# Kernel optimization log

Measured on AMD Instinct MI355X. Metric: run time of the kernel, lower is better.

## Reference

```python
import jax, jax.numpy as jnp
import numpy as np

NODE_DIM = 256
EDGE_DIM = 128
HIDDEN = EDGE_DIM // 2  # edge_downsample=2 -> 64
LN_EPS = 1e-5


def setup_inputs() -> dict:
    key = jax.random.key(0)
    ks = jax.random.split(key, 12)
    B, N = 1, 768
    s_in = 1.0 / np.sqrt(NODE_DIM)
    s_h = 1.0 / np.sqrt(HIDDEN)
    return {
        "x": jax.random.normal(ks[0], (B, N, NODE_DIM), jnp.float32),
        "z": jnp.zeros((1,), jnp.float32),  # unused in forward (matches torch module)
        "Wi": jax.random.uniform(ks[1], (NODE_DIM, HIDDEN), jnp.float32, -s_in, s_in),
        "bi": jax.random.uniform(ks[2], (HIDDEN,), jnp.float32, -s_in, s_in),
        "Wj": jax.random.uniform(ks[3], (NODE_DIM, HIDDEN), jnp.float32, -s_in, s_in),
        "bj": jax.random.uniform(ks[4], (HIDDEN,), jnp.float32, -s_in, s_in),
        "ln_g": jnp.ones((HIDDEN,), jnp.float32),
        "ln_b": jnp.zeros((HIDDEN,), jnp.float32),
        "W1": jax.random.uniform(ks[5], (HIDDEN, HIDDEN), jnp.float32, -s_h, s_h),
        "b1": jax.random.uniform(ks[6], (HIDDEN,), jnp.float32, -s_h, s_h),
        "W2": jax.random.uniform(ks[7], (HIDDEN, EDGE_DIM), jnp.float32, -s_h, s_h),
        "b2": jax.random.uniform(ks[8], (EDGE_DIM,), jnp.float32, -s_h, s_h),
    }


def _layernorm(h, g, b):
    mu = jnp.mean(h, axis=-1, keepdims=True)
    var = jnp.mean(jnp.square(h - mu), axis=-1, keepdims=True)
    return (h - mu) * jax.lax.rsqrt(var + LN_EPS) * g + b


def reference(x, z, Wi, bi, Wj, bj, ln_g, ln_b, W1, b1, W2, b2):
    # x: [B, N, node_dim]
    n_i = x @ Wi + bi  # [B, N, H]
    n_j = x @ Wj + bj  # [B, N, H]
    # outer sum: [B, N(j-axis first per torch indexing), N, H]
    n_in = n_i[:, None, :, :] + n_j[:, :, None, :]
    h = _layernorm(n_in, ln_g, ln_b)
    h = jax.nn.relu(h @ W1 + b1)
    return h @ W2 + b2  # [B, N, N, edge_dim]
```

## Files before the change

### kernel.cpp

```cpp
#include <hip/hip_runtime.h>
#include <hip/hip_bf16.h>

typedef float f32x4 __attribute__((ext_vector_type(4)));
typedef short s16x8 __attribute__((ext_vector_type(8)));
typedef short s16x4 __attribute__((ext_vector_type(4)));

#define N_NODES 768
#define NODE_DIM_ 256
#define HDIM 64
#define EDIM 128
#define CTILES 48
#define TILES_TOTAL (N_NODES * CTILES)

static __device__ __forceinline__ short f2bf(float f) {
    __hip_bfloat16 h = __float2bfloat16(f);
    return __builtin_bit_cast(short, h);
}

__global__ __launch_bounds__(256) void proj_kernel(
        const float* __restrict__ x,
        const float* __restrict__ Wi, const float* __restrict__ bi,
        const float* __restrict__ Wj, const float* __restrict__ bj,
        float* __restrict__ NI, float* __restrict__ NJ) {
    int row  = blockIdx.x * 4 + (threadIdx.x >> 6);
    int lane = threadIdx.x & 63;
    float ai = bi[lane];
    float aj = bj[lane];
    const float* xr = x + row * NODE_DIM_;
#pragma unroll 8
    for (int k = 0; k < NODE_DIM_; ++k) {
        float xv = xr[k];
        ai = fmaf(xv, Wi[k * HDIM + lane], ai);
        aj = fmaf(xv, Wj[k * HDIM + lane], aj);
    }
    NI[row * HDIM + lane] = ai;
    NJ[row * HDIM + lane] = aj;
}

__global__ __launch_bounds__(256) void edge_kernel(
        const float* __restrict__ NI, const float* __restrict__ NJ,
        const float* __restrict__ lng, const float* __restrict__ lnb,
        const float* __restrict__ W1, const float* __restrict__ b1,
        const float* __restrict__ W2, const float* __restrict__ b2,
        float* __restrict__ out) {
    __shared__ short W1L[4096];
    __shared__ short W2L[8192];
    __shared__ short TL[4][1024];

    for (int idx = threadIdx.x; idx < 4096; idx += 256) {
        int k = idx >> 6, n = idx & 63;
        W1L[(k >> 3) * 512 + n * 8 + (k & 7)] = f2bf(W1[idx]);
    }
    for (int idx = threadIdx.x; idx < 8192; idx += 256) {
        int k = idx >> 7, n = idx & 127;
        W2L[(k >> 3) * 1024 + n * 8 + (k & 7)] = f2bf(W2[idx]);
    }
    __syncthreads();

    const int wave = threadIdx.x >> 6;
    const int lane = threadIdx.x & 63;
    const int l15  = lane & 15;
    const int hi   = lane >> 4;
    const int swz  = (l15 & 7) << 4;

    float gl[8], gh[8], bl[8], bh[8];
#pragma unroll
    for (int j = 0; j < 8; ++j) {
        gl[j] = lng[hi * 8 + j];      gh[j] = lng[32 + hi * 8 + j];
        bl[j] = lnb[hi * 8 + j];      bh[j] = lnb[32 + hi * 8 + j];
    }
    float b1v[16];
#pragma unroll
    for (int nt = 0; nt < 4; ++nt)
#pragma unroll
        for (int r = 0; r < 4; ++r)
            b1v[nt * 4 + r] = b1[nt * 16 + hi * 4 + r];
    float b2v[8];
#pragma unroll
    for (int nt = 0; nt < 8; ++nt)
        b2v[nt] = b2[nt * 16 + l15];

    char* tl = (char*)&TL[wave][0];

    const int wid = blockIdx.x * 4 + wave;
    const int nw  = gridDim.x * 4;
    for (int t = wid; t < TILES_TOTAL; t += nw) {
        int a  = t / CTILES;
        int c0 = (t - a * CTILES) * 16;

        const float* nip = NI + (c0 + l15) * HDIM + hi * 8;
        const float* njp = NJ + a * HDIM + hi * 8;
        float v[16];
#pragma unroll
        for (int j = 0; j < 8; ++j) {
            v[j]     = nip[j]      + njp[j];
            v[8 + j] = nip[32 + j] + njp[32 + j];
        }
        float s = 0.f, ss = 0.f;
#pragma unroll
        for (int j = 0; j < 16; ++j) { s += v[j]; ss = fmaf(v[j], v[j], ss); }
        s += __shfl_xor(s, 16);  ss += __shfl_xor(ss, 16);
        s += __shfl_xor(s, 32);  ss += __shfl_xor(ss, 32);
        float mu   = s * (1.f / 64.f);
        float var  = ss * (1.f / 64.f) - mu * mu;
        float rstd = rsqrtf(var + 1e-5f);

        s16x8 hf0, hf1;
#pragma unroll
        for (int j = 0; j < 8; ++j) {
            hf0[j] = f2bf(fmaf((v[j]     - mu) * rstd, gl[j], bl[j]));
            hf1[j] = f2bf(fmaf((v[8 + j] - mu) * rstd, gh[j], bh[j]));
        }

#pragma unroll
        for (int nt = 0; nt < 4; ++nt) {
            f32x4 acc = {0.f, 0.f, 0.f, 0.f};
            s16x8 w0 = *(const s16x8*)&W1L[(0 + hi) * 512 + (nt * 16 + l15) * 8];
            s16x8 w1 = *(const s16x8*)&W1L[(4 + hi) * 512 + (nt * 16 + l15) * 8];
            acc = __builtin_amdgcn_mfma_f32_16x16x32_bf16(w0, hf0, acc, 0, 0, 0);
            acc = __builtin_amdgcn_mfma_f32_16x16x32_bf16(w1, hf1, acc, 0, 0, 0);
            s16x4 tv;
#pragma unroll
            for (int r = 0; r < 4; ++r)
                tv[r] = f2bf(fmaxf(acc[r] + b1v[nt * 4 + r], 0.f));
            int wb = (l15 * 128 + (nt * 16 + hi * 4) * 2) ^ swz;
            *(s16x4*)(tl + wb) = tv;
        }

        int rb0 = (l15 * 128 + hi * 16) ^ swz;
        int rb1 = (l15 * 128 + hi * 16 + 64) ^ swz;
        s16x8 tf0 = *(const s16x8*)(tl + rb0);
        s16x8 tf1 = *(const s16x8*)(tl + rb1);

        float* op = out + ((size_t)(a * N_NODES + c0 + hi * 4)) * EDIM + l15;
#pragma unroll
        for (int nt = 0; nt < 8; ++nt) {
            f32x4 acc = {0.f, 0.f, 0.f, 0.f};
            s16x8 w0 = *(const s16x8*)&W2L[(0 + hi) * 1024 + (nt * 16 + l15) * 8];
            s16x8 w1 = *(const s16x8*)&W2L[(4 + hi) * 1024 + (nt * 16 + l15) * 8];
            acc = __builtin_amdgcn_mfma_f32_16x16x32_bf16(tf0, w0, acc, 0, 0, 0);
            acc = __builtin_amdgcn_mfma_f32_16x16x32_bf16(tf1, w1, acc, 0, 0, 0);
#pragma unroll
            for (int r = 0; r < 4; ++r)
                op[(size_t)r * EDIM + nt * 16] = acc[r] + b2v[nt];
        }
    }
}

extern "C" void kernel_launch(void* const* d_in, const int* in_sizes, int n_in,
                              void* d_out, int out_size, void* d_ws, size_t ws_size,
                              hipStream_t stream) {
    const float* x   = (const float*)d_in[0];
    const float* Wi  = (const float*)d_in[2];
    const float* bi  = (const float*)d_in[3];
    const float* Wj  = (const float*)d_in[4];
    const float* bj  = (const float*)d_in[5];
    const float* lng = (const float*)d_in[6];
    const float* lnb = (const float*)d_in[7];
    const float* W1  = (const float*)d_in[8];
    const float* b1  = (const float*)d_in[9];
    const float* W2  = (const float*)d_in[10];
    const float* b2  = (const float*)d_in[11];
    float* out = (float*)d_out;

    float* NI = (float*)d_ws;
    float* NJ = NI + N_NODES * HDIM;

    proj_kernel<<<N_NODES / 4, 256, 0, stream>>>(x, Wi, bi, Wj, bj, NI, NJ);
    edge_kernel<<<2304, 256, 0, stream>>>(NI, NJ, lng, lnb, W1, b1, W2, b2, out);
}
```

Before: 80.91 us.

## Fold LayerNorm and first linear layer into per-node precomputed projections

The first MLP layer after LayerNorm is rewritten algebraically. Per-node projections through gamma-scaled W1 (Pi, Pj), row means and second moments, and the column sums S1 and bias C1 are precomputed in the projection kernel. The edge kernel then gets mean and variance from per-node stats plus one dot product, and forms the hidden activations with a few FMAs. This removes the first MFMA stage, the LDS staging, and W1 loading. Each wave now owns a fixed column tile and iterates over 12 row tiles with 768 blocks. The risk is the numerical precision of computing variance from moments, and the kernel is still dominated by the large output write.

```diff
diff --git a/kernel.cpp b/kernel.cpp
--- a/kernel.cpp
+++ b/kernel.cpp
@@ -3,14 +3,13 @@
 
 typedef float f32x4 __attribute__((ext_vector_type(4)));
 typedef short s16x8 __attribute__((ext_vector_type(8)));
-typedef short s16x4 __attribute__((ext_vector_type(4)));
 
 #define N_NODES 768
 #define NODE_DIM_ 256
 #define HDIM 64
 #define EDIM 128
 #define CTILES 48
-#define TILES_TOTAL (N_NODES * CTILES)
+#define ATILES_PER_WAVE 12
 
 static __device__ __forceinline__ short f2bf(float f) {
     __hip_bfloat16 h = __float2bfloat16(f);
@@ -21,11 +20,23 @@
         const float* __restrict__ x,
         const float* __restrict__ Wi, const float* __restrict__ bi,
         const float* __restrict__ Wj, const float* __restrict__ bj,
-        float* __restrict__ NI, float* __restrict__ NJ) {
-    int row  = blockIdx.x * 4 + (threadIdx.x >> 6);
-    int lane = threadIdx.x & 63;
-    float ai = bi[lane];
-    float aj = bj[lane];
+        const float* __restrict__ W1, const float* __restrict__ b1,
+        const float* __restrict__ lng, const float* __restrict__ lnb,
+        float* __restrict__ NI, float* __restrict__ NJ,
+        float* __restrict__ Pi, float* __restrict__ Pj,
+        float* __restrict__ mi, float* __restrict__ qi,
+        float* __restrict__ mj, float* __restrict__ qj,
+        float* __restrict__ S1, float* __restrict__ C1) {
+    __shared__ float W1gL[HDIM * HDIM];
+    __shared__ float rowi[4][HDIM], rowj[4][HDIM];
+    for (int idx = threadIdx.x; idx < HDIM * HDIM; idx += 256) {
+        int k = idx >> 6;
+        W1gL[idx] = lng[k] * W1[idx];
+    }
+
+    int wave = threadIdx.x >> 6, lane = threadIdx.x & 63;
+    int row  = blockIdx.x * 4 + wave;
+    float ai = bi[lane], aj = bj[lane];
     const float* xr = x + row * NODE_DIM_;
 #pragma unroll 8
     for (int k = 0; k < NODE_DIM_; ++k) {
@@ -35,25 +46,56 @@
     }
     NI[row * HDIM + lane] = ai;
     NJ[row * HDIM + lane] = aj;
-}
-
-__global__ __launch_bounds__(256) void edge_kernel(
+    rowi[wave][lane] = ai;
+    rowj[wave][lane] = aj;
+
+    float si = ai, sqi = ai * ai, sj = aj, sqj = aj * aj;
+#pragma unroll
+    for (int o = 1; o < 64; o <<= 1) {
+        si  += __shfl_xor(si, o);   sqi += __shfl_xor(sqi, o);
+        sj  += __shfl_xor(sj, o);   sqj += __shfl_xor(sqj, o);
+    }
+    if (lane == 0) {
+        mi[row] = si * (1.f / 64.f);  qi[row] = sqi * (1.f / 64.f);
+        mj[row] = sj * (1.f / 64.f);  qj[row] = sqj * (1.f / 64.f);
+    }
+    __syncthreads();
+
+    float pi = 0.f, pj = 0.f;
+#pragma unroll 8
+    for (int k = 0; k < HDIM; ++k) {
+        float wg = W1gL[k * HDIM + lane];
+        pi = fmaf(rowi[wave][k], wg, pi);
+        pj = fmaf(rowj[wave][k], wg, pj);
+    }
+    Pi[row * HDIM + lane] = pi;
+    Pj[row * HDIM + lane] = pj;
+
+    if (blockIdx.x == 0 && threadIdx.x < HDIM) {
+        int n = threadIdx.x;
+        float s = 0.f, cc = 0.f;
+#pragma unroll 8
+        for (int k = 0; k < HDIM; ++k) {
+            s += W1gL[k * HDIM + n];
+            cc = fmaf(lnb[k], W1[k * HDIM + n], cc);
+        }
+        S1[n] = s;
+        C1[n] = cc + b1[n];
+    }
+}
+
+__global__ __launch_bounds__(256, 3) void edge_kernel(
         const float* __restrict__ NI, const float* __restrict__ NJ,
-        const float* __restrict__ lng, const float* __restrict__ lnb,
-        const float* __restrict__ W1, const float* __restrict__ b1,
+        const float* __restrict__ Pi, const float* __restrict__ Pj,
+        const float* __restrict__ mi, const float* __restrict__ qi,
+        const float* __restrict__ mj, const float* __restrict__ qj,
+        const float* __restrict__ S1, const float* __restrict__ C1,
         const float* __restrict__ W2, const float* __restrict__ b2,
         float* __restrict__ out) {
-    __shared__ short W1L[4096];
     __shared__ short W2L[8192];
-    __shared__ short TL[4][1024];
-
-    for (int idx = threadIdx.x; idx < 4096; idx += 256) {
-        int k = idx >> 6, n = idx & 63;
-        W1L[(k >> 3) * 512 + n * 8 + (k & 7)] = f2bf(W1[idx]);
-    }
     for (int idx = threadIdx.x; idx < 8192; idx += 256) {
-        int k = idx >> 7, n = idx & 127;
-        W2L[(k >> 3) * 1024 + n * 8 + (k & 7)] = f2bf(W2[idx]);
+        int k = idx >> 7, e = idx & 127;
+        W2L[(k >> 3) * 1024 + e * 8 + (k & 7)] = f2bf(W2[idx]);
     }
     __syncthreads();
 
@@ -61,76 +103,80 @@
     const int lane = threadIdx.x & 63;
     const int l15  = lane & 15;
     const int hi   = lane >> 4;
-    const int swz  = (l15 & 7) << 4;
-
-    float gl[8], gh[8], bl[8], bh[8];
-#pragma unroll
-    for (int j = 0; j < 8; ++j) {
-        gl[j] = lng[hi * 8 + j];      gh[j] = lng[32 + hi * 8 + j];
-        bl[j] = lnb[hi * 8 + j];      bh[j] = lnb[32 + hi * 8 + j];
-    }
-    float b1v[16];
-#pragma unroll
-    for (int nt = 0; nt < 4; ++nt)
-#pragma unroll
-        for (int r = 0; r < 4; ++r)
-            b1v[nt * 4 + r] = b1[nt * 16 + hi * 4 + r];
+
+    const int wid     = blockIdx.x * 4 + wave;
+    const int c0      = (wid % CTILES) * 16;
+    const int a_start = wid / CTILES;
+    const int c       = c0 + l15;
+
+    const float* nip = NI + c * HDIM + hi * 8;
+    f32x4 vi0 = *(const f32x4*)nip;
+    f32x4 vi1 = *(const f32x4*)(nip + 4);
+    f32x4 vi2 = *(const f32x4*)(nip + 32);
+    f32x4 vi3 = *(const f32x4*)(nip + 36);
+    const float* pip = Pi + c * HDIM + hi * 8;
+    f32x4 pia = *(const f32x4*)pip;
+    f32x4 pib = *(const f32x4*)(pip + 4);
+    f32x4 pic = *(const f32x4*)(pip + 32);
+    f32x4 pid = *(const f32x4*)(pip + 36);
+    const float mic = mi[c], qic = qi[c];
+    f32x4 S1a = *(const f32x4*)&S1[hi * 8];
+    f32x4 S1b = *(const f32x4*)&S1[hi * 8 + 4];
+    f32x4 S1c = *(const f32x4*)&S1[32 + hi * 8];
+    f32x4 S1d = *(const f32x4*)&S1[32 + hi * 8 + 4];
+    f32x4 C1a = *(const f32x4*)&C1[hi * 8];
+    f32x4 C1b = *(const f32x4*)&C1[hi * 8 + 4];
+    f32x4 C1c = *(const f32x4*)&C1[32 + hi * 8];
+    f32x4 C1d = *(const f32x4*)&C1[32 + hi * 8 + 4];
     float b2v[8];
 #pragma unroll
     for (int nt = 0; nt < 8; ++nt)
         b2v[nt] = b2[nt * 16 + l15];
 
-    char* tl = (char*)&TL[wave][0];
-
-    const int wid = blockIdx.x * 4 + wave;
-    const int nw  = gridDim.x * 4;
-    for (int t = wid; t < TILES_TOTAL; t += nw) {
-        int a  = t / CTILES;
-        int c0 = (t - a * CTILES) * 16;
-
-        const float* nip = NI + (c0 + l15) * HDIM + hi * 8;
+#pragma unroll 2
+    for (int ai = 0; ai < ATILES_PER_WAVE; ++ai) {
+        const int a = a_start + ai * 64;
+
         const float* njp = NJ + a * HDIM + hi * 8;
-        float v[16];
-#pragma unroll
-        for (int j = 0; j < 8; ++j) {
-            v[j]     = nip[j]      + njp[j];
-            v[8 + j] = nip[32 + j] + njp[32 + j];
-        }
-        float s = 0.f, ss = 0.f;
-#pragma unroll
-        for (int j = 0; j < 16; ++j) { s += v[j]; ss = fmaf(v[j], v[j], ss); }
-        s += __shfl_xor(s, 16);  ss += __shfl_xor(ss, 16);
-        s += __shfl_xor(s, 32);  ss += __shfl_xor(ss, 32);
-        float mu   = s * (1.f / 64.f);
-        float var  = ss * (1.f / 64.f) - mu * mu;
-        float rstd = rsqrtf(var + 1e-5f);
-
-        s16x8 hf0, hf1;
-#pragma unroll
-        for (int j = 0; j < 8; ++j) {
-            hf0[j] = f2bf(fmaf((v[j]     - mu) * rstd, gl[j], bl[j]));
-            hf1[j] = f2bf(fmaf((v[8 + j] - mu) * rstd, gh[j], bh[j]));
-        }
-
-#pragma unroll
-        for (int nt = 0; nt < 4; ++nt) {
-            f32x4 acc = {0.f, 0.f, 0.f, 0.f};
-            s16x8 w0 = *(const s16x8*)&W1L[(0 + hi) * 512 + (nt * 16 + l15) * 8];
-            s16x8 w1 = *(const s16x8*)&W1L[(4 + hi) * 512 + (nt * 16 + l15) * 8];
-            acc = __builtin_amdgcn_mfma_f32_16x16x32_bf16(w0, hf0, acc, 0, 0, 0);
-            acc = __builtin_amdgcn_mfma_f32_16x16x32_bf16(w1, hf1, acc, 0, 0, 0);
-            s16x4 tv;
-#pragma unroll
-            for (int r = 0; r < 4; ++r)
-                tv[r] = f2bf(fmaxf(acc[r] + b1v[nt * 4 + r], 0.f));
-            int wb = (l15 * 128 + (nt * 16 + hi * 4) * 2) ^ swz;
-            *(s16x4*)(tl + wb) = tv;
-        }
-
-        int rb0 = (l15 * 128 + hi * 16) ^ swz;
-        int rb1 = (l15 * 128 + hi * 16 + 64) ^ swz;
-        s16x8 tf0 = *(const s16x8*)(tl + rb0);
-        s16x8 tf1 = *(const s16x8*)(tl + rb1);
+        f32x4 nj0 = *(const f32x4*)njp;
+        f32x4 nj1 = *(const f32x4*)(njp + 4);
+        f32x4 nj2 = *(const f32x4*)(njp + 32);
+        f32x4 nj3 = *(const f32x4*)(njp + 36);
+        const float* pjp = Pj + a * HDIM + hi * 8;
+        f32x4 pj0 = *(const f32x4*)pjp;
+        f32x4 pj1 = *(const f32x4*)(pjp + 4);
+        f32x4 pj2 = *(const f32x4*)(pjp + 32);
+        f32x4 pj3 = *(const f32x4*)(pjp + 36);
+        const float mja = mj[a], qja = qj[a];
+
+        float d = 0.f;
+#pragma unroll
+        for (int j = 0; j < 4; ++j) {
+            d = fmaf(vi0[j], nj0[j], d);
+            d = fmaf(vi1[j], nj1[j], d);
+            d = fmaf(vi2[j], nj2[j], d);
+            d = fmaf(vi3[j], nj3[j], d);
+        }
+        d += __shfl_xor(d, 16);
+        d += __shfl_xor(d, 32);
+
+        const float mu   = mic + mja;
+        const float var  = qic + qja + d * (1.f / 32.f) - mu * mu;
+        const float rstd = rsqrtf(var + 1e-5f);
+        const float rm   = rstd * mu;
+
+        s16x8 tf0, tf1;
+#pragma unroll
+        for (int j = 0; j < 4; ++j) {
+            float t0 = fmaf(rstd, pia[j] + pj0[j], fmaf(-rm, S1a[j], C1a[j]));
+            float t1 = fmaf(rstd, pib[j] + pj1[j], fmaf(-rm, S1b[j], C1b[j]));
+            float t2 = fmaf(rstd, pic[j] + pj2[j], fmaf(-rm, S1c[j], C1c[j]));
+            float t3 = fmaf(rstd, pid[j] + pj3[j], fmaf(-rm, S1d[j], C1d[j]));
+            tf0[j]     = f2bf(fmaxf(t0, 0.f));
+            tf0[4 + j] = f2bf(fmaxf(t1, 0.f));
+            tf1[j]     = f2bf(fmaxf(t2, 0.f));
+            tf1[4 + j] = f2bf(fmaxf(t3, 0.f));
+        }
 
         float* op = out + ((size_t)(a * N_NODES + c0 + hi * 4)) * EDIM + l15;
 #pragma unroll
@@ -163,9 +209,20 @@
     const float* b2  = (const float*)d_in[11];
     float* out = (float*)d_out;
 
-    float* NI = (float*)d_ws;
-    float* NJ = NI + N_NODES * HDIM;
-
-    proj_kernel<<<N_NODES / 4, 256, 0, stream>>>(x, Wi, bi, Wj, bj, NI, NJ);
-    edge_kernel<<<2304, 256, 0, stream>>>(NI, NJ, lng, lnb, W1, b1, W2, b2, out);
-}
+    float* ws = (float*)d_ws;
+    float* NI = ws;
+    float* NJ = NI + 49152;
+    float* Pi = NJ + 49152;
+    float* Pj = Pi + 49152;
+    float* mi = Pj + 49152;
+    float* qi = mi + 768;
+    float* mj = qi + 768;
+    float* qj = mj + 768;
+    float* S1 = qj + 768;
+    float* C1 = S1 + 64;
+
+    proj_kernel<<<N_NODES / 4, 256, 0, stream>>>(x, Wi, bi, Wj, bj, W1, b1, lng, lnb,
+                                                 NI, NJ, Pi, Pj, mi, qi, mj, qj, S1, C1);
+    edge_kernel<<<768, 256, 0, stream>>>(NI, NJ, Pi, Pj, mi, qi, mj, qj,
+                                         S1, C1, W2, b2, out);
+}
```

New measurement: 127.9 us. 58.0% more time.

## Split activations into bf16 hi/lo pairs and remap tiles to contiguous per-wave chunks

Applied to the files above, without the earlier changes.

Activations feeding both MFMA stages are split into a bf16 high part and a bf16 residual low part, and each product is accumulated twice. This doubles MFMA work and LDS traffic for the activations to get higher accuracy, which looks like a response to a tolerance failure. The grid-stride tile loop is also replaced by a fixed assignment of four consecutive tiles per wave, with a block-index swizzle across XCDs to improve locality. The new mapping assumes a grid of exactly 2304 blocks.

```diff
diff --git a/kernel.cpp b/kernel.cpp
--- a/kernel.cpp
+++ b/kernel.cpp
@@ -15,6 +15,10 @@
 static __device__ __forceinline__ short f2bf(float f) {
     __hip_bfloat16 h = __float2bfloat16(f);
     return __builtin_bit_cast(short, h);
+}
+static __device__ __forceinline__ float bf2f(short h) {
+    unsigned u = ((unsigned)(unsigned short)h) << 16;
+    return __builtin_bit_cast(float, u);
 }
 
 __global__ __launch_bounds__(256) void proj_kernel(
@@ -45,7 +49,8 @@
         float* __restrict__ out) {
     __shared__ short W1L[4096];
     __shared__ short W2L[8192];
-    __shared__ short TL[4][1024];
+    __shared__ short TLh[4][1024];
+    __shared__ short TLl[4][1024];
 
     for (int idx = threadIdx.x; idx < 4096; idx += 256) {
         int k = idx >> 6, n = idx & 63;
@@ -80,13 +85,18 @@
     for (int nt = 0; nt < 8; ++nt)
         b2v[nt] = b2[nt * 16 + l15];
 
-    char* tl = (char*)&TL[wave][0];
+    char* tlh = (char*)&TLh[wave][0];
+    char* tll = (char*)&TLl[wave][0];
 
-    const int wid = blockIdx.x * 4 + wave;
-    const int nw  = gridDim.x * 4;
-    for (int t = wid; t < TILES_TOTAL; t += nw) {
-        int a  = t / CTILES;
-        int c0 = (t - a * CTILES) * 16;
+    const int swzb = (blockIdx.x & 7) * 288 + (blockIdx.x >> 3);
+    const int wid  = swzb * 4 + wave;
+    const int t0   = wid * 4;
+
+#pragma unroll 1
+    for (int k4 = 0; k4 < 4; ++k4) {
+        const int t  = t0 + k4;
+        const int a  = t / CTILES;
+        const int c0 = (t - a * CTILES) * 16;
 
         const float* nip = NI + (c0 + l15) * HDIM + hi * 8;
         const float* njp = NJ + a * HDIM + hi * 8;
@@ -105,11 +115,15 @@
         float var  = ss * (1.f / 64.f) - mu * mu;
         float rstd = rsqrtf(var + 1e-5f);
 
-        s16x8 hf0, hf1;
+        s16x8 hf0h, hf0l, hf1h, hf1l;
 #pragma unroll
         for (int j = 0; j < 8; ++j) {
-            hf0[j] = f2bf(fmaf((v[j]     - mu) * rstd, gl[j], bl[j]));
-            hf1[j] = f2bf(fmaf((v[8 + j] - mu) * rstd, gh[j], bh[j]));
+            float h0 = fmaf((v[j]     - mu) * rstd, gl[j], bl[j]);
+            float h1 = fmaf((v[8 + j] - mu) * rstd, gh[j], bh[j]);
+            short a0 = f2bf(h0);
+            short a1 = f2bf(h1);
+            hf0h[j] = a0;  hf0l[j] = f2bf(h0 - bf2f(a0));
+            hf1h[j] = a1;  hf1l[j] = f2bf(h1 - bf2f(a1));
         }
 
 #pragma unroll
@@ -117,20 +131,29 @@
             f32x4 acc = {0.f, 0.f, 0.f, 0.f};
             s16x8 w0 = *(const s16x8*)&W1L[(0 + hi) * 512 + (nt * 16 + l15) * 8];
             s16x8 w1 = *(const s16x8*)&W1L[(4 + hi) * 512 + (nt * 16 + l15) * 8];
-            acc = __builtin_amdgcn_mfma_f32_16x16x32_bf16(w0, hf0, acc, 0, 0, 0);
-            acc = __builtin_amdgcn_mfma_f32_16x16x32_bf16(w1, hf1, acc, 0, 0, 0);
-            s16x4 tv;
+            acc = __builtin_amdgcn_mfma_f32_16x16x32_bf16(w0, hf0h, acc, 0, 0, 0);
+            acc = __builtin_amdgcn_mfma_f32_16x16x32_bf16(w1, hf1h, acc, 0, 0, 0);
+            acc = __builtin_amdgcn_mfma_f32_16x16x32_bf16(w0, hf0l, acc, 0, 0, 0);
+            acc = __builtin_amdgcn_mfma_f32_16x16x32_bf16(w1, hf1l, acc, 0, 0, 0);
+            s16x4 tvh, tvl;
 #pragma unroll
-            for (int r = 0; r < 4; ++r)
-                tv[r] = f2bf(fmaxf(acc[r] + b1v[nt * 4 + r], 0.f));
+            for (int r = 0; r < 4; ++r) {
+                float tt = fmaxf(acc[r] + b1v[nt * 4 + r], 0.f);
+                short th = f2bf(tt);
+                tvh[r] = th;
+                tvl[r] = f2bf(tt - bf2f(th));
+            }
             int wb = (l15 * 128 + (nt * 16 + hi * 4) * 2) ^ swz;
-            *(s16x4*)(tl + wb) = tv;
+            *(s16x4*)(tlh + wb) = tvh;
+            *(s16x4*)(tll + wb) = tvl;
         }
 
         int rb0 = (l15 * 128 + hi * 16) ^ swz;
         int rb1 = (l15 * 128 + hi * 16 + 64) ^ swz;
-        s16x8 tf0 = *(const s16x8*)(tl + rb0);
-        s16x8 tf1 = *(const s16x8*)(tl + rb1);
+        s16x8 tf0h = *(const s16x8*)(tlh + rb0);
+        s16x8 tf1h = *(const s16x8*)(tlh + rb1);
+        s16x8 tf0l = *(const s16x8*)(tll + rb0);
+        s16x8 tf1l = *(const s16x8*)(tll + rb1);
 
         float* op = out + ((size_t)(a * N_NODES + c0 + hi * 4)) * EDIM + l15;
 #pragma unroll
@@ -138,8 +161,10 @@
             f32x4 acc = {0.f, 0.f, 0.f, 0.f};
             s16x8 w0 = *(const s16x8*)&W2L[(0 + hi) * 1024 + (nt * 16 + l15) * 8];
             s16x8 w1 = *(const s16x8*)&W2L[(4 + hi) * 1024 + (nt * 16 + l15) * 8];
-            acc = __builtin_amdgcn_mfma_f32_16x16x32_bf16(tf0, w0, acc, 0, 0, 0);
-            acc = __builtin_amdgcn_mfma_f32_16x16x32_bf16(tf1, w1, acc, 0, 0, 0);
+            acc = __builtin_amdgcn_mfma_f32_16x16x32_bf16(tf0h, w0, acc, 0, 0, 0);
+            acc = __builtin_amdgcn_mfma_f32_16x16x32_bf16(tf1h, w1, acc, 0, 0, 0);
+            acc = __builtin_amdgcn_mfma_f32_16x16x32_bf16(tf0l, w0, acc, 0, 0, 0);
+            acc = __builtin_amdgcn_mfma_f32_16x16x32_bf16(tf1l, w1, acc, 0, 0, 0);
 #pragma unroll
             for (int r = 0; r < 4; ++r)
                 op[(size_t)r * EDIM + nt * 16] = acc[r] + b2v[nt];
```

Result: slower. 89.80 us (+11.0%).
